# Kernel tuning notes

Hardware: AMD Instinct MI355X
Metric: run time of the kernel (lower is better)

The kernel has to match this reference:

```python
import jax, jax.numpy as jnp
import numpy as np

N_NODES = 50000
N_EDGES = 800000
N_GRAPHS = 64
NEG_SLOPE = 0.2  # PyG GATConv default leaky_relu slope
EPS = 1e-16      # PyG softmax denominator epsilon


def gat_conv(x, W, a_src, a_dst, bias, src, dst, n_nodes):
    """PyG GATConv (heads=1, concat=True, self-loops already appended).
    x: [N, F_in], W: [F_in, H*F], a_src/a_dst: [H, F], bias: [H*F]."""
    H, F = a_src.shape
    h = (x @ W).reshape(-1, H, F)                      # [N, H, F]
    alpha_src = jnp.einsum('nhf,hf->nh', h, a_src)     # [N, H]
    alpha_dst = jnp.einsum('nhf,hf->nh', h, a_dst)     # [N, H]
    e = jax.nn.leaky_relu(alpha_src[src] + alpha_dst[dst], NEG_SLOPE)  # [E, H]
    # segment softmax over incoming edges of each destination node
    e_max = jax.ops.segment_max(e, dst, num_segments=n_nodes)          # [N, H]
    e_exp = jnp.exp(e - e_max[dst])
    denom = jax.ops.segment_sum(e_exp, dst, num_segments=n_nodes)      # [N, H]
    alpha = e_exp / (denom[dst] + EPS)                                 # [E, H]
    msg = alpha[:, :, None] * h[src]                                   # [E, H, F]
    out = jax.ops.segment_sum(msg, dst, num_segments=n_nodes)          # [N, H, F]
    return out.reshape(-1, H * F) + bias


def global_mean_pool(x, batch, n_graphs):
    s = jax.ops.segment_sum(x, batch, num_segments=n_graphs)
    cnt = jax.ops.segment_sum(jnp.ones((x.shape[0],), x.dtype), batch, num_segments=n_graphs)
    return s / jnp.maximum(cnt, 1.0)[:, None]


def setup_inputs() -> dict:
    key = jax.random.key(0)
    ks = jax.random.split(key, 10)
    d_in, d_h, d_out, L, H = 128, 128, 10, 3, 1
    x = jax.random.normal(ks[0], (N_NODES, d_in), dtype=jnp.float32)
    edge_index = jax.random.randint(ks[1], (2, N_EDGES), 0, N_NODES, dtype=jnp.int32)
    edge_attr = jax.random.normal(ks[2], (N_EDGES, 4), dtype=jnp.float32)
    batch = jnp.sort(jax.random.randint(ks[3], (N_NODES,), 0, N_GRAPHS, dtype=jnp.int32))
    s0 = 1.0 / np.sqrt(d_in)
    sh = 1.0 / np.sqrt(d_h)
    return {
        'x': x,
        'edge_index': edge_index,
        'edge_attr': edge_attr,
        'batch': batch,
        'W0': jax.random.normal(ks[4], (d_in, d_h), dtype=jnp.float32) * s0,
        'b0': jnp.zeros((d_h,), jnp.float32),
        'Wc': jax.random.normal(ks[5], (L, d_h, H * d_h), dtype=jnp.float32) * sh,
        'att_src': jax.random.normal(ks[6], (L, H, d_h), dtype=jnp.float32) * sh,
        'att_dst': jax.random.normal(ks[7], (L, H, d_h), dtype=jnp.float32) * sh,
        'bc': jnp.zeros((L, H * d_h), jnp.float32),
        'W1': jax.random.normal(ks[8], (d_h, d_out), dtype=jnp.float32) * sh,
        'b1': jnp.zeros((d_out,), jnp.float32),
    }


def reference(x, edge_index, edge_attr, batch, W0, b0, Wc, att_src, att_dst, bc, W1, b1):
    n = x.shape[0]
    # GATConv default add_self_loops=True
    loops = jnp.arange(n, dtype=edge_index.dtype)
    src = jnp.concatenate([edge_index[0], loops])
    dst = jnp.concatenate([edge_index[1], loops])
    # dropout p=0 / eval mode -> identity
    h = jax.nn.relu(x @ W0 + b0)
    for i in range(Wc.shape[0]):
        h = jax.nn.relu(gat_conv(h, Wc[i], att_src[i], att_dst[i], bc[i], src, dst, n))
    pooled = global_mean_pool(h, batch, N_GRAPHS)   # [B, d_h]
    return pooled @ W1 + b1                          # [B, d_out]
```

## Files before the change

### kernel.cpp

```cpp
#include <hip/hip_runtime.h>
#include <hip/hip_bf16.h>
#include <hip/hip_fp16.h>
#include <hip/hip_fp8.h>

#define NN 50000
#define NE 800000
#define NG 64
#define DH 128

#define NPB 256
#define NBK ((NN + NPB - 1) / NPB)
#define EPB 4096
#define NPBLK ((NE + EPB - 1) / EPB)
#define CAPB 5120
#define GEMMB 512
#define GEMMW (GEMMB * 4)
#define CST 136
#define CSTB 136
#define SMEM_BYTES 18432

#if defined(__has_builtin)
# if __has_builtin(__builtin_amdgcn_cvt_pk_f32_fp8) && __has_builtin(__builtin_amdgcn_cvt_pk_fp8_f32)
#  define HW_FP8 1
# endif
#endif

typedef __bf16 bfx8 __attribute__((ext_vector_type(8)));
typedef float  f32x4 __attribute__((ext_vector_type(4)));
typedef float  f32x8 __attribute__((ext_vector_type(8)));

__device__ __forceinline__ ushort f2b(float f) {
    unsigned b = __float_as_uint(f);
    b += 0x7fff + ((b >> 16) & 1);
    return (ushort)(b >> 16);
}
__device__ __forceinline__ float b2f(ushort s) {
    return __uint_as_float((unsigned)s << 16);
}
__device__ __forceinline__ unsigned pk2(float a, float b) {
    return (unsigned)f2b(a) | ((unsigned)f2b(b) << 16);
}

__device__ __forceinline__ unsigned f2fp8(float v) {
    v = fminf(fmaxf(v, -448.f), 448.f);
#ifdef HW_FP8
    return (unsigned)__builtin_amdgcn_cvt_pk_fp8_f32(v, v, 0, false) & 0xFFu;
#else
    __hip_fp8_e4m3 t(v);
    return (unsigned)*(const unsigned char*)&t;
#endif
}
__device__ __forceinline__ void fp8x4_up(unsigned u, float* o) {
#ifdef HW_FP8
    auto lo = __builtin_amdgcn_cvt_pk_f32_fp8((int)u, false);
    auto hi = __builtin_amdgcn_cvt_pk_f32_fp8((int)u, true);
    o[0] = lo[0]; o[1] = lo[1]; o[2] = hi[0]; o[3] = hi[1];
#else
    #pragma unroll
    for (int k = 0; k < 4; ++k) {
        unsigned char c = (u >> (8 * k)) & 0xFF;
        o[k] = float(*(const __hip_fp8_e4m3*)&c);
    }
#endif
}

__launch_bounds__(256)
__global__ void k_partwt(const int* __restrict__ ei, int* __restrict__ gcur,
                         unsigned* __restrict__ tmp,
                         const float* __restrict__ W0, const float* __restrict__ Wc,
                         ushort* __restrict__ Wt) {
    int t = threadIdx.x;
    if (blockIdx.x >= NPBLK) {
        int i = (blockIdx.x - NPBLK) * 256 + t;
        int m = i >> 14;
        int r = i & 16383;
        int k = r >> 7, n = r & 127;
        const float* src = (m == 0) ? W0 : (Wc + (size_t)(m - 1) * DH * DH);
        Wt[(size_t)m * DH * DH + n * DH + k] = f2b(src[r]);
        return;
    }
    __shared__ int cnt[NBK], base[NBK], lcur[NBK];
    for (int i = t; i < NBK; i += 256) cnt[i] = 0;
    __syncthreads();
    int e0 = blockIdx.x * EPB;
    int dreg[16];
    #pragma unroll
    for (int j = 0; j < 16; ++j) {
        int e = e0 + j * 256 + t;
        dreg[j] = (e < NE) ? ei[NE + e] : -1;
        if (e < NE) atomicAdd(&cnt[dreg[j] >> 8], 1);
    }
    __syncthreads();
    for (int i = t; i < NBK; i += 256) {
        base[i] = cnt[i] ? atomicAdd(&gcur[i], cnt[i]) : 0;
        lcur[i] = 0;
    }
    __syncthreads();
    #pragma unroll
    for (int j = 0; j < 16; ++j) {
        int e = e0 + j * 256 + t;
        if (e < NE) {
            int d = dreg[j], s = ei[e];
            int b = d >> 8;
            int r = atomicAdd(&lcur[b], 1);
            tmp[(size_t)b * CAPB + base[b] + r] = ((unsigned)(d & 255) << 16) | (unsigned)s;
        }
    }
}

__launch_bounds__(256)
__global__ void k_bcount(const unsigned* __restrict__ tmp, const int* __restrict__ gcur,
                         int* __restrict__ deg, int* __restrict__ ploc,
                         int* __restrict__ bsizeP) {
    __shared__ int dcnt[NPB];
    int b = blockIdx.x, t = threadIdx.x;
    dcnt[t] = 0;
    __syncthreads();
    int ne = gcur[b];
    for (int e = t; e < ne; e += 256)
        atomicAdd(&dcnt[tmp[(size_t)b * CAPB + e] >> 16], 1);
    __syncthreads();
    int n = b * NPB + t;
    int d = (n < NN) ? dcnt[t] : 0;
    int p = (n < NN) ? ((d + 4) & ~3) : 0;
    int inc = p;
    #pragma unroll
    for (int off = 1; off < 64; off <<= 1) {
        int u = __shfl_up(inc, off);
        if ((t & 63) >= off) inc += u;
    }
    __shared__ int wsum[4];
    if ((t & 63) == 63) wsum[t >> 6] = inc;
    __syncthreads();
    int w = t >> 6, woff = 0;
    #pragma unroll
    for (int k = 0; k < 4; ++k) if (k < w) woff += wsum[k];
    int lofs = inc - p + woff;
    if (n < NN) { deg[n] = d; ploc[n] = lofs; }
    if (t == 255) bsizeP[b] = lofs + p;
}

template<bool AF32, bool DOTS, bool OUTFP8>
__device__ __forceinline__ void gemm_body(char* smem, int gblk,
        const void* __restrict__ Av, const ushort* __restrict__ Wt,
        const float* __restrict__ bias, void* __restrict__ C, int relu,
        const float* __restrict__ avs, const float* __restrict__ avd,
        float* __restrict__ asrc, float* __restrict__ adst) {
    const int NT = NN / 16;
    int tid = threadIdx.x;
    int lane = tid & 63;
    int mrow = lane & 15;
    int quad = lane >> 4;
    int wid = (gblk * 256 + tid) >> 6;

    bfx8 b[4][8];
    #pragma unroll
    for (int ks = 0; ks < 4; ++ks) {
        int k0 = ks * 32 + quad * 8;
        #pragma unroll
        for (int t = 0; t < 8; ++t)
            b[ks][t] = *(const bfx8*)(Wt + (size_t)(t * 16 + mrow) * DH + k0);
    }
    float av[8], dv[8];
    if (DOTS) {
        #pragma unroll
        for (int t = 0; t < 8; ++t) {
            av[t] = avs[t * 16 + mrow];
            dv[t] = avd[t * 16 + mrow];
        }
    }

    for (int tile = wid; tile < NT; tile += GEMMW) {
        int row0 = tile * 16;
        int arow = row0 + mrow;

        bfx8 a[4];
        if (AF32) {
            f32x8 af[4];
            #pragma unroll
            for (int ks = 0; ks < 4; ++ks)
                af[ks] = *(const f32x8*)((const float*)Av + (size_t)arow * DH + ks * 32 + quad * 8);
            #pragma unroll
            for (int ks = 0; ks < 4; ++ks) {
                union { ushort s[8]; bfx8 v; } u;
                #pragma unroll
                for (int j = 0; j < 8; ++j) u.s[j] = f2b(af[ks][j]);
                a[ks] = u.v;
            }
        } else {
            #pragma unroll
            for (int ks = 0; ks < 4; ++ks)
                a[ks] = *(const bfx8*)((const ushort*)Av + (size_t)arow * DH + ks * 32 + quad * 8);
        }

        f32x4 acc[8];
        #pragma unroll
        for (int t = 0; t < 8; ++t)
            #pragma unroll
            for (int r = 0; r < 4; ++r) acc[t][r] = 0.f;

        #pragma unroll
        for (int ks = 0; ks < 4; ++ks)
            #pragma unroll
            for (int t = 0; t < 8; ++t)
                acc[t] = __builtin_amdgcn_mfma_f32_16x16x32_bf16(a[ks], b[ks][t], acc[t], 0, 0, 0);

        if (OUTFP8) {
            uchar* my = (uchar*)smem + (tid >> 6) * 16 * CSTB;
            #pragma unroll
            for (int t = 0; t < 8; ++t) {
                int col = t * 16 + mrow;
                float bv = bias ? bias[col] : 0.f;
                #pragma unroll
                for (int r = 0; r < 4; ++r) {
                    float v = acc[t][r] + bv;
                    if (relu) v = fmaxf(v, 0.f);
                    my[(quad * 4 + r) * CSTB + col] = (uchar)f2fp8(v);
                }
            }
            #pragma unroll
            for (int i = 0; i < 4; ++i) {
                int idx = i * 64 + lane;
                int row = idx >> 4;
                int c8 = idx & 15;
                uint2 u = *(const uint2*)(my + row * CSTB + c8 * 8);
                *(uint2*)((uchar*)C + (size_t)(row0 + row) * DH + c8 * 8) = u;
            }
        } else {
            ushort* my = (ushort*)smem + (tid >> 6) * 16 * CST;
            #pragma unroll
            for (int t = 0; t < 8; ++t) {
                int col = t * 16 + mrow;
                float bv = bias ? bias[col] : 0.f;
                #pragma unroll
                for (int r = 0; r < 4; ++r) {
                    float v = acc[t][r] + bv;
                    if (relu) v = fmaxf(v, 0.f);
                    my[(quad * 4 + r) * CST + col] = f2b(v);
                }
            }
            #pragma unroll
            for (int i = 0; i < 4; ++i) {
                int idx = i * 64 + lane;
                int row = idx >> 4;
                int c16 = idx & 15;
                uint4 u = *(const uint4*)(my + row * CST + c16 * 8);
                *(uint4*)((ushort*)C + (size_t)(row0 + row) * DH + c16 * 8) = u;
            }
        }

        if (DOTS) {
            int orow = row0 + quad * 4;
            #pragma unroll
            for (int r = 0; r < 4; ++r) {
                float ps = 0.f, pd = 0.f;
                #pragma unroll
                for (int t = 0; t < 8; ++t) {
                    ps += acc[t][r] * av[t];
                    pd += acc[t][r] * dv[t];
                }
                #pragma unroll
                for (int off = 1; off < 16; off <<= 1) {
                    ps += __shfl_xor(ps, off);
                    pd += __shfl_xor(pd, off);
                }
                if (mrow == 0) {
                    asrc[orow + r] = ps;
                    adst[orow + r] = pd;
                }
            }
        }
    }
}

__launch_bounds__(256)
__global__ void k_buildgemm(const unsigned* __restrict__ tmp, const int* __restrict__ gcur,
                            const int* __restrict__ bsizeP, const int* __restrict__ ploc,
                            int* __restrict__ pstart, ushort* __restrict__ csr,
                            const float* __restrict__ x, const ushort* __restrict__ Wt,
                            const float* __restrict__ b0, ushort* __restrict__ hB) {
    __shared__ char smem[SMEM_BYTES];
    int t = threadIdx.x;
    if (blockIdx.x < GEMMB) {
        gemm_body<true, false, false>(smem, blockIdx.x, x, Wt, b0, hB, 1,
                                      nullptr, nullptr, nullptr, nullptr);
        return;
    }
    int b = blockIdx.x - GEMMB;
    ushort* buf = (ushort*)smem;
    int* lcur = (int*)(smem + 16384);
    int* sm   = (int*)(smem + 16384 + 1024);
    int v = (t < NBK) ? bsizeP[t] : 0;
    sm[t] = v;
    __syncthreads();
    for (int off = 1; off < 256; off <<= 1) {
        int u = (t >= off) ? sm[t - off] : 0;
        __syncthreads();
        sm[t] += u;
        __syncthreads();
    }
    int r0 = sm[b] - bsizeP[b];
    int S = bsizeP[b];
    int n0 = b * NPB, n1 = min(n0 + NPB, NN), nodes = n1 - n0;
    int ne = gcur[b];

    if (S <= 8192) {
        for (int i = t; i < (S >> 1); i += 256) ((unsigned*)buf)[i] = 0;
        __syncthreads();
        if (t < nodes) {
            int lp = ploc[n0 + t];
            pstart[n0 + t] = r0 + lp;
            lcur[t] = lp + 1;
            buf[lp] = (ushort)(n0 + t);
        }
        __syncthreads();
        for (int e = t; e < ne; e += 256) {
            unsigned u = tmp[(size_t)b * CAPB + e];
            int slot = atomicAdd(&lcur[u >> 16], 1);
            buf[slot] = (ushort)(u & 0xffffu);
        }
        __syncthreads();
        unsigned* dst = (unsigned*)(csr + r0);
        for (int i = t; i < (S >> 1); i += 256) dst[i] = ((unsigned*)buf)[i];
    } else {
        for (int i = t; i < S; i += 256) csr[r0 + i] = 0;
        __syncthreads();
        if (t < nodes) {
            int lp = ploc[n0 + t];
            pstart[n0 + t] = r0 + lp;
            lcur[t] = r0 + lp + 1;
            csr[r0 + lp] = (ushort)(n0 + t);
        }
        __syncthreads();
        for (int e = t; e < ne; e += 256) {
            unsigned u = tmp[(size_t)b * CAPB + e];
            int slot = atomicAdd(&lcur[u >> 16], 1);
            csr[slot] = (ushort)(u & 0xffffu);
        }
    }
}

__launch_bounds__(256)
__global__ void k_gemmdots(const ushort* __restrict__ hB, const ushort* __restrict__ Wt,
                           uchar* __restrict__ hA,
                           const float* __restrict__ avs, const float* __restrict__ avd,
                           float* __restrict__ asrc, float* __restrict__ adst) {
    __shared__ char smem[SMEM_BYTES];
    gemm_body<false, true, true>(smem, blockIdx.x, hB, Wt, nullptr, hA, 0,
                                 avs, avd, asrc, adst);
}

__launch_bounds__(256)
__global__ void k_aggr(const uchar* __restrict__ h8, const float* __restrict__ asrc,
                       const float* __restrict__ adst, const int* __restrict__ pstart,
                       const int* __restrict__ deg, const ushort* __restrict__ csr,
                       const float* __restrict__ bias, ushort* __restrict__ hout) {
    int wid = (blockIdx.x * blockDim.x + threadIdx.x) >> 6;
    int lane = threadIdx.x & 63;
    if (wid >= NN) return;
    int start = pstart[wid];
    int cnt = deg[wid] + 1;
    float ad = adst[wid];

    if (cnt <= 64) {
        int s = csr[start + lane];
        float e = -1e30f;
        if (lane < cnt) {
            float t = asrc[s] + ad;
            e = fmaxf(t, 0.f) + 0.2f * fminf(t, 0.f);
        }
        float m = e;
        #pragma unroll
        for (int off = 32; off; off >>= 1) m = fmaxf(m, __shfl_xor(m, off));
        float w = (lane < cnt) ? __expf(e - m) : 0.f;
        float dsum = w;
        #pragma unroll
        for (int off = 32; off; off >>= 1) dsum += __shfl_xor(dsum, off);

        int g = lane >> 4, fidx = lane & 15;
        float acc[8];
        #pragma unroll
        for (int k = 0; k < 8; ++k) acc[k] = 0.f;

        int steps = (cnt + 3) >> 2;
        const uint2* hp = (const uint2*)h8;
        int j = 0;
        for (; j + 3 < steps; j += 4) {
            int   e0 = j * 4 + g,      e1 = e0 + 4,  e2 = e0 + 8,  e3 = e0 + 12;
            float w0 = __shfl(w, e0),  w1 = __shfl(w, e1);
            float w2 = __shfl(w, e2),  w3 = __shfl(w, e3);
            int   s0 = __shfl(s, e0),  s1 = __shfl(s, e1);
            int   s2 = __shfl(s, e2),  s3 = __shfl(s, e3);
            uint2 u0 = hp[(size_t)s0 * 16 + fidx];
            uint2 u1 = hp[(size_t)s1 * 16 + fidx];
            uint2 u2 = hp[(size_t)s2 * 16 + fidx];
            uint2 u3 = hp[(size_t)s3 * 16 + fidx];
            float v[8];
            fp8x4_up(u0.x, v); fp8x4_up(u0.y, v + 4);
            #pragma unroll
            for (int k = 0; k < 8; ++k) acc[k] += w0 * v[k];
            fp8x4_up(u1.x, v); fp8x4_up(u1.y, v + 4);
            #pragma unroll
            for (int k = 0; k < 8; ++k) acc[k] += w1 * v[k];
            fp8x4_up(u2.x, v); fp8x4_up(u2.y, v + 4);
            #pragma unroll
            for (int k = 0; k < 8; ++k) acc[k] += w2 * v[k];
            fp8x4_up(u3.x, v); fp8x4_up(u3.y, v + 4);
            #pragma unroll
            for (int k = 0; k < 8; ++k) acc[k] += w3 * v[k];
        }
        for (; j < steps; ++j) {
            int e0 = j * 4 + g;
            float w0 = __shfl(w, e0);
            int   s0 = __shfl(s, e0);
            uint2 u0 = hp[(size_t)s0 * 16 + fidx];
            float v[8];
            fp8x4_up(u0.x, v); fp8x4_up(u0.y, v + 4);
            #pragma unroll
            for (int k = 0; k < 8; ++k) acc[k] += w0 * v[k];
        }
        #pragma unroll
        for (int k = 0; k < 8; ++k) {
            acc[k] += __shfl_xor(acc[k], 16);
            acc[k] += __shfl_xor(acc[k], 32);
        }
        if (g == 0) {
            float inv = 1.f / (dsum + 1e-16f);
            const float4* bp = (const float4*)bias;
            float4 b0 = bp[fidx * 2], b1 = bp[fidx * 2 + 1];
            uint4 o;
            o.x = pk2(fmaxf(acc[0] * inv + b0.x, 0.f), fmaxf(acc[1] * inv + b0.y, 0.f));
            o.y = pk2(fmaxf(acc[2] * inv + b0.z, 0.f), fmaxf(acc[3] * inv + b0.w, 0.f));
            o.z = pk2(fmaxf(acc[4] * inv + b1.x, 0.f), fmaxf(acc[5] * inv + b1.y, 0.f));
            o.w = pk2(fmaxf(acc[6] * inv + b1.z, 0.f), fmaxf(acc[7] * inv + b1.w, 0.f));
            ((uint4*)hout)[(size_t)wid * 16 + fidx] = o;
        }
        return;
    }

    float m = -1e30f;
    for (int i0 = start; i0 < start + cnt; i0 += 64) {
        int i = i0 + lane;
        float e = -1e30f;
        if (i < start + cnt) {
            int s = csr[i];
            float t = asrc[s] + ad;
            e = fmaxf(t, 0.f) + 0.2f * fminf(t, 0.f);
        }
        m = fmaxf(m, e);
    }
    #pragma unroll
    for (int off = 32; off; off >>= 1) m = fmaxf(m, __shfl_xor(m, off));

    float accx = 0.f, accy = 0.f, dsum = 0.f;
    for (int i0 = start; i0 < start + cnt; i0 += 64) {
        int i = i0 + lane;
        int s = 0; float w = 0.f;
        if (i < start + cnt) {
            s = csr[i];
            float t = asrc[s] + ad;
            float e = fmaxf(t, 0.f) + 0.2f * fminf(t, 0.f);
            w = __expf(e - m);
        }
        dsum += w;
        int cl = min(64, start + cnt - i0);
        for (int j = 0; j < cl; ++j) {
            int   sj = __shfl(s, j);
            float wj = __shfl(w, j);
            unsigned us = *(const ushort*)(h8 + (size_t)sj * DH + lane * 2);
            float v[4];
            fp8x4_up(us, v);
            accx += wj * v[0];
            accy += wj * v[1];
        }
    }
    #pragma unroll
    for (int off = 32; off; off >>= 1) dsum += __shfl_xor(dsum, off);

    float inv = 1.f / (dsum + 1e-16f);
    float ox = fmaxf(accx * inv + bias[lane * 2], 0.f);
    float oy = fmaxf(accy * inv + bias[lane * 2 + 1], 0.f);
    *(unsigned*)(hout + (size_t)wid * DH + lane * 2) = pk2(ox, oy);
}

__launch_bounds__(256)
__global__ void k_pool(const ushort* __restrict__ h, const int* __restrict__ batch,
                       float* __restrict__ gsum, int* __restrict__ gcnt) {
    int slot = threadIdx.x >> 7;
    int f = threadIdx.x & 127;
    int n0 = blockIdx.x * 64;
    int n1 = min(n0 + 64, NN);
    int first = n0 + slot;
    if (first >= n1) return;
    int g0 = batch[n0], g1 = batch[n1 - 1];
    if (g0 == g1) {
        float acc = 0.f;
        for (int nd = first; nd < n1; nd += 2)
            acc += b2f(h[(size_t)nd * DH + f]);
        atomicAdd(&gsum[g0 * DH + f], acc);
        if (f == 0 && slot == 0) atomicAdd(&gcnt[g0], n1 - n0);
        return;
    }
    float acc = 0.f; int run = 0;
    int gcur = batch[first];
    for (int nd = first; nd < n1; nd += 2) {
        int g = batch[nd];
        if (g != gcur) {
            atomicAdd(&gsum[gcur * DH + f], acc);
            if (f == 0) atomicAdd(&gcnt[gcur], run);
            acc = 0.f; run = 0; gcur = g;
        }
        acc += b2f(h[(size_t)nd * DH + f]);
        run += 1;
    }
    atomicAdd(&gsum[gcur * DH + f], acc);
    if (f == 0) atomicAdd(&gcnt[gcur], run);
}

__global__ void k_final(const float* __restrict__ gsum, const int* __restrict__ gcnt,
                        const float* __restrict__ W1, const float* __restrict__ b1,
                        float* __restrict__ out) {
    int t = threadIdx.x;
    if (t >= NG * 10) return;
    int g = t / 10, o = t % 10;
    float inv = 1.f / fmaxf((float)gcnt[g], 1.f);
    float acc = 0.f;
    for (int f = 0; f < DH; ++f) acc += gsum[g * DH + f] * W1[f * 10 + o];
    out[t] = acc * inv + b1[o];
}

extern "C" void kernel_launch(void* const* d_in, const int* in_sizes, int n_in,
                              void* d_out, int out_size, void* d_ws, size_t ws_size,
                              hipStream_t stream) {
    const float* x       = (const float*)d_in[0];
    const int*   ei      = (const int*)d_in[1];
    const int*   batch   = (const int*)d_in[3];
    const float* W0      = (const float*)d_in[4];
    const float* b0      = (const float*)d_in[5];
    const float* Wc      = (const float*)d_in[6];
    const float* att_src = (const float*)d_in[7];
    const float* att_dst = (const float*)d_in[8];
    const float* bc      = (const float*)d_in[9];
    const float* W1      = (const float*)d_in[10];
    const float* b1      = (const float*)d_in[11];
    float* out = (float*)d_out;

    char* ws = (char*)d_ws;
    size_t off = 0;
    auto alloc = [&](size_t bytes) {
        void* p = ws + off;
        off += (bytes + 255) & ~(size_t)255;
        return p;
    };
    uchar*    hA     = (uchar*)alloc((size_t)NN * DH);
    ushort*   hB     = (ushort*)alloc((size_t)NN * DH * 2);
    ushort*   Wt     = (ushort*)alloc((size_t)4 * DH * DH * 2);
    int*      pstart = (int*)alloc((size_t)NN * 4);
    ushort*   csr    = (ushort*)alloc((size_t)(NE + 4 * NN + 64) * 2);
    unsigned* tmp    = (unsigned*)alloc((size_t)NBK * CAPB * 4);
    float*    asrc   = (float*)alloc(NN * 4);
    float*    adst   = (float*)alloc(NN * 4);
    int*      deg    = (int*)alloc(NN * 4);
    int*      ploc   = (int*)alloc(NN * 4);
    int*      gcur   = (int*)alloc((NBK + 1) * 4);
    int*      bsizeP = (int*)alloc((NBK + 1) * 4);
    float*    gsum   = (float*)alloc(NG * DH * 4);
    int*      gcnt   = (int*)alloc(NG * 4);

    hipMemsetAsync(gcur, 0, (NBK + 1) * 4, stream);
    hipMemsetAsync(gsum, 0, NG * DH * 4 + 256, stream);

    k_partwt<<<NPBLK + 256, 256, 0, stream>>>(ei, gcur, tmp, W0, Wc, Wt);
    k_bcount<<<NBK, 256, 0, stream>>>(tmp, gcur, deg, ploc, bsizeP);
    k_buildgemm<<<GEMMB + NBK, 256, 0, stream>>>(tmp, gcur, bsizeP, ploc, pstart, csr,
                                                 x, Wt, b0, hB);

    for (int l = 0; l < 3; ++l) {
        k_gemmdots<<<GEMMB, 256, 0, stream>>>(hB, Wt + (size_t)(l + 1) * DH * DH, hA,
                                              att_src + l * DH, att_dst + l * DH,
                                              asrc, adst);
        k_aggr<<<(NN + 3) / 4, 256, 0, stream>>>(hA, asrc, adst, pstart, deg, csr,
                                                 bc + l * DH, hB);
    }

    k_pool<<<(NN + 63) / 64, 256, 0, stream>>>(hB, batch, gsum, gcnt);
    k_final<<<1, NG * 10, 0, stream>>>(gsum, gcnt, W1, b1, out);
}
```

Measured before the change: 309.2 us.

## Process two nodes per wavefront in aggregation and count degrees during partitioning

```diff
diff --git a/kernel.cpp b/kernel.cpp
--- a/kernel.cpp
+++ b/kernel.cpp
@@ -18,6 +18,7 @@
 #define CST 136
 #define CSTB 136
 #define SMEM_BYTES 18432
+#define NPAIR (NN / 2)
 
 #if defined(__has_builtin)
 # if __has_builtin(__builtin_amdgcn_cvt_pk_f32_fp8) && __has_builtin(__builtin_amdgcn_cvt_pk_fp8_f32)
@@ -66,7 +67,7 @@
 
 __launch_bounds__(256)
 __global__ void k_partwt(const int* __restrict__ ei, int* __restrict__ gcur,
-                         unsigned* __restrict__ tmp,
+                         unsigned* __restrict__ tmp, int* __restrict__ deg,
                          const float* __restrict__ W0, const float* __restrict__ Wc,
                          ushort* __restrict__ Wt) {
     int t = threadIdx.x;
@@ -88,7 +89,10 @@
     for (int j = 0; j < 16; ++j) {
         int e = e0 + j * 256 + t;
         dreg[j] = (e < NE) ? ei[NE + e] : -1;
-        if (e < NE) atomicAdd(&cnt[dreg[j] >> 8], 1);
+        if (e < NE) {
+            atomicAdd(&cnt[dreg[j] >> 8], 1);
+            atomicAdd(&deg[dreg[j]], 1);
+        }
     }
     __syncthreads();
     for (int i = t; i < NBK; i += 256) {
@@ -109,19 +113,11 @@
 }
 
 __launch_bounds__(256)
-__global__ void k_bcount(const unsigned* __restrict__ tmp, const int* __restrict__ gcur,
-                         int* __restrict__ deg, int* __restrict__ ploc,
+__global__ void k_bcount(const int* __restrict__ deg, int* __restrict__ ploc,
                          int* __restrict__ bsizeP) {
-    __shared__ int dcnt[NPB];
     int b = blockIdx.x, t = threadIdx.x;
-    dcnt[t] = 0;
-    __syncthreads();
-    int ne = gcur[b];
-    for (int e = t; e < ne; e += 256)
-        atomicAdd(&dcnt[tmp[(size_t)b * CAPB + e] >> 16], 1);
-    __syncthreads();
     int n = b * NPB + t;
-    int d = (n < NN) ? dcnt[t] : 0;
+    int d = (n < NN) ? deg[n] : 0;
     int p = (n < NN) ? ((d + 4) & ~3) : 0;
     int inc = p;
     #pragma unroll
@@ -136,7 +132,7 @@
     #pragma unroll
     for (int k = 0; k < 4; ++k) if (k < w) woff += wsum[k];
     int lofs = inc - p + woff;
-    if (n < NN) { deg[n] = d; ploc[n] = lofs; }
+    if (n < NN) ploc[n] = lofs;
     if (t == 255) bsizeP[b] = lofs + p;
 }
 
@@ -350,14 +346,11 @@
                                  avs, avd, asrc, adst);
 }
 
-__launch_bounds__(256)
-__global__ void k_aggr(const uchar* __restrict__ h8, const float* __restrict__ asrc,
-                       const float* __restrict__ adst, const int* __restrict__ pstart,
-                       const int* __restrict__ deg, const ushort* __restrict__ csr,
-                       const float* __restrict__ bias, ushort* __restrict__ hout) {
-    int wid = (blockIdx.x * blockDim.x + threadIdx.x) >> 6;
-    int lane = threadIdx.x & 63;
-    if (wid >= NN) return;
+__device__ __forceinline__ void aggr_one(int wid, int lane,
+        const uchar* __restrict__ h8, const float* __restrict__ asrc,
+        const float* __restrict__ adst, const int* __restrict__ pstart,
+        const int* __restrict__ deg, const ushort* __restrict__ csr,
+        const float* __restrict__ bias, ushort* __restrict__ hout) {
     int start = pstart[wid];
     int cnt = deg[wid] + 1;
     float ad = adst[wid];
@@ -384,32 +377,7 @@
 
         int steps = (cnt + 3) >> 2;
         const uint2* hp = (const uint2*)h8;
-        int j = 0;
-        for (; j + 3 < steps; j += 4) {
-            int   e0 = j * 4 + g,      e1 = e0 + 4,  e2 = e0 + 8,  e3 = e0 + 12;
-            float w0 = __shfl(w, e0),  w1 = __shfl(w, e1);
-            float w2 = __shfl(w, e2),  w3 = __shfl(w, e3);
-            int   s0 = __shfl(s, e0),  s1 = __shfl(s, e1);
-            int   s2 = __shfl(s, e2),  s3 = __shfl(s, e3);
-            uint2 u0 = hp[(size_t)s0 * 16 + fidx];
-            uint2 u1 = hp[(size_t)s1 * 16 + fidx];
-            uint2 u2 = hp[(size_t)s2 * 16 + fidx];
-            uint2 u3 = hp[(size_t)s3 * 16 + fidx];
-            float v[8];
-            fp8x4_up(u0.x, v); fp8x4_up(u0.y, v + 4);
-            #pragma unroll
-            for (int k = 0; k < 8; ++k) acc[k] += w0 * v[k];
-            fp8x4_up(u1.x, v); fp8x4_up(u1.y, v + 4);
-            #pragma unroll
-            for (int k = 0; k < 8; ++k) acc[k] += w1 * v[k];
-            fp8x4_up(u2.x, v); fp8x4_up(u2.y, v + 4);
-            #pragma unroll
-            for (int k = 0; k < 8; ++k) acc[k] += w2 * v[k];
-            fp8x4_up(u3.x, v); fp8x4_up(u3.y, v + 4);
-            #pragma unroll
-            for (int k = 0; k < 8; ++k) acc[k] += w3 * v[k];
-        }
-        for (; j < steps; ++j) {
+        for (int j = 0; j < steps; ++j) {
             int e0 = j * 4 + g;
             float w0 = __shfl(w, e0);
             int   s0 = __shfl(s, e0);
@@ -481,6 +449,99 @@
     float ox = fmaxf(accx * inv + bias[lane * 2], 0.f);
     float oy = fmaxf(accy * inv + bias[lane * 2 + 1], 0.f);
     *(unsigned*)(hout + (size_t)wid * DH + lane * 2) = pk2(ox, oy);
+}
+
+__launch_bounds__(256)
+__global__ void k_aggr(const uchar* __restrict__ h8, const float* __restrict__ asrc,
+                       const float* __restrict__ adst, const int* __restrict__ pstart,
+                       const int* __restrict__ deg, const ushort* __restrict__ csr,
+                       const float* __restrict__ bias, ushort* __restrict__ hout) {
+    int pid = (blockIdx.x * blockDim.x + threadIdx.x) >> 6;
+    int lane = threadIdx.x & 63;
+    if (pid >= NPAIR) return;
+    int half = lane >> 5, hl = lane & 31;
+    int nd = pid * 2 + half;
+
+    int cnt = deg[nd] + 1;
+    int cother = __shfl_xor(cnt, 32);
+    if (max(cnt, cother) <= 32) {
+        int start = pstart[nd];
+        float ad = adst[nd];
+        int s = csr[start + hl];
+        float e = -1e30f;
+        if (hl < cnt) {
+            float t = asrc[s] + ad;
+            e = fmaxf(t, 0.f) + 0.2f * fminf(t, 0.f);
+        }
+        float m = e;
+        #pragma unroll
+        for (int off = 16; off; off >>= 1) m = fmaxf(m, __shfl_xor(m, off));
+        float w = (hl < cnt) ? __expf(e - m) : 0.f;
+        float dsum = w;
+        #pragma unroll
+        for (int off = 16; off; off >>= 1) dsum += __shfl_xor(dsum, off);
+
+        int g = hl >> 4, fidx = hl & 15;
+        int lbase = half * 32;
+        float acc[8];
+        #pragma unroll
+        for (int k = 0; k < 8; ++k) acc[k] = 0.f;
+
+        int steps = (cnt + 1) >> 1;
+        const uint2* hp = (const uint2*)h8;
+        int j = 0;
+        for (; j + 3 < steps; j += 4) {
+            int   e0 = j * 2 + g,       e1 = e0 + 2, e2 = e0 + 4, e3 = e0 + 6;
+            float w0 = __shfl(w, lbase + e0), w1 = __shfl(w, lbase + e1);
+            float w2 = __shfl(w, lbase + e2), w3 = __shfl(w, lbase + e3);
+            int   s0 = __shfl(s, lbase + e0), s1 = __shfl(s, lbase + e1);
+            int   s2 = __shfl(s, lbase + e2), s3 = __shfl(s, lbase + e3);
+            uint2 u0 = hp[(size_t)s0 * 16 + fidx];
+            uint2 u1 = hp[(size_t)s1 * 16 + fidx];
+            uint2 u2 = hp[(size_t)s2 * 16 + fidx];
+            uint2 u3 = hp[(size_t)s3 * 16 + fidx];
+            float v[8];
+            fp8x4_up(u0.x, v); fp8x4_up(u0.y, v + 4);
+            #pragma unroll
+            for (int k = 0; k < 8; ++k) acc[k] += w0 * v[k];
+            fp8x4_up(u1.x, v); fp8x4_up(u1.y, v + 4);
+            #pragma unroll
+            for (int k = 0; k < 8; ++k) acc[k] += w1 * v[k];
+            fp8x4_up(u2.x, v); fp8x4_up(u2.y, v + 4);
+            #pragma unroll
+            for (int k = 0; k < 8; ++k) acc[k] += w2 * v[k];
+            fp8x4_up(u3.x, v); fp8x4_up(u3.y, v + 4);
+            #pragma unroll
+            for (int k = 0; k < 8; ++k) acc[k] += w3 * v[k];
+        }
+        for (; j < steps; ++j) {
+            int   e0 = j * 2 + g;
+            float w0 = __shfl(w, lbase + e0);
+            int   s0 = __shfl(s, lbase + e0);
+            uint2 u0 = hp[(size_t)s0 * 16 + fidx];
+            float v[8];
+            fp8x4_up(u0.x, v); fp8x4_up(u0.y, v + 4);
+            #pragma unroll
+            for (int k = 0; k < 8; ++k) acc[k] += w0 * v[k];
+        }
+        #pragma unroll
+        for (int k = 0; k < 8; ++k) acc[k] += __shfl_xor(acc[k], 16);
+        if (g == 0) {
+            float inv = 1.f / (dsum + 1e-16f);
+            const float4* bp = (const float4*)bias;
+            float4 b0 = bp[fidx * 2], b1 = bp[fidx * 2 + 1];
+            uint4 o;
+            o.x = pk2(fmaxf(acc[0] * inv + b0.x, 0.f), fmaxf(acc[1] * inv + b0.y, 0.f));
+            o.y = pk2(fmaxf(acc[2] * inv + b0.z, 0.f), fmaxf(acc[3] * inv + b0.w, 0.f));
+            o.z = pk2(fmaxf(acc[4] * inv + b1.x, 0.f), fmaxf(acc[5] * inv + b1.y, 0.f));
+            o.w = pk2(fmaxf(acc[6] * inv + b1.z, 0.f), fmaxf(acc[7] * inv + b1.w, 0.f));
+            ((uint4*)hout)[(size_t)nd * 16 + fidx] = o;
+        }
+        return;
+    }
+
+    aggr_one(pid * 2,     lane, h8, asrc, adst, pstart, deg, csr, bias, hout);
+    aggr_one(pid * 2 + 1, lane, h8, asrc, adst, pstart, deg, csr, bias, hout);
 }
 
 __launch_bounds__(256)
@@ -561,17 +622,17 @@
     float*    asrc   = (float*)alloc(NN * 4);
     float*    adst   = (float*)alloc(NN * 4);
     int*      deg    = (int*)alloc(NN * 4);
+    int*      gcur   = (int*)alloc((NBK + 1) * 4);
     int*      ploc   = (int*)alloc(NN * 4);
-    int*      gcur   = (int*)alloc((NBK + 1) * 4);
     int*      bsizeP = (int*)alloc((NBK + 1) * 4);
     float*    gsum   = (float*)alloc(NG * DH * 4);
     int*      gcnt   = (int*)alloc(NG * 4);
 
-    hipMemsetAsync(gcur, 0, (NBK + 1) * 4, stream);
+    hipMemsetAsync(deg, 0, 200192 + (NBK + 1) * 4, stream);
     hipMemsetAsync(gsum, 0, NG * DH * 4 + 256, stream);
 
-    k_partwt<<<NPBLK + 256, 256, 0, stream>>>(ei, gcur, tmp, W0, Wc, Wt);
-    k_bcount<<<NBK, 256, 0, stream>>>(tmp, gcur, deg, ploc, bsizeP);
+    k_partwt<<<NPBLK + 256, 256, 0, stream>>>(ei, gcur, tmp, deg, W0, Wc, Wt);
+    k_bcount<<<NBK, 256, 0, stream>>>(deg, ploc, bsizeP);
     k_buildgemm<<<GEMMB + NBK, 256, 0, stream>>>(tmp, gcur, bsizeP, ploc, pstart, csr,
                                                  x, Wt, b0, hB);
 
@@ -579,8 +640,8 @@
         k_gemmdots<<<GEMMB, 256, 0, stream>>>(hB, Wt + (size_t)(l + 1) * DH * DH, hA,
                                               att_src + l * DH, att_dst + l * DH,
                                               asrc, adst);
-        k_aggr<<<(NN + 3) / 4, 256, 0, stream>>>(hA, asrc, adst, pstart, deg, csr,
-                                                 bc + l * DH, hB);
+        k_aggr<<<(NPAIR + 3) / 4, 256, 0, stream>>>(hA, asrc, adst, pstart, deg, csr,
+                                                    bc + l * DH, hB);
     }
 
     k_pool<<<(NN + 63) / 64, 256, 0, stream>>>(hB, batch, gsum, gcnt);
```

After: 315.3 us. About the same (+2.0%).
